# Kernel tuning notes

Measured on AMD Instinct MI355X. Metric: run time of the kernel, lower is better.

## Reference

```python
import jax, jax.numpy as jnp
import numpy as np

B, S, H = 4, 512, 1024
E, K, I = 8, 2, 2048

def setup_inputs() -> dict:
    key = jax.random.key(0)
    k1, k2, k3, k4, k5 = jax.random.split(key, 5)
    scale_h = 1.0 / np.sqrt(H)
    scale_i = 1.0 / np.sqrt(I)
    return {
        "hidden_states": jax.random.normal(k1, (B, S, H), dtype=jnp.float32),
        "router_w": jax.random.normal(k2, (E, H), dtype=jnp.float32) * scale_h,
        "w_gate": jax.random.normal(k3, (E, H, I), dtype=jnp.float32) * scale_h,
        "w_up": jax.random.normal(k4, (E, H, I), dtype=jnp.float32) * scale_h,
        "w_down": jax.random.normal(k5, (E, I, H), dtype=jnp.float32) * scale_i,
    }

def reference(hidden_states, router_w, w_gate, w_up, w_down):
    b, s, h = hidden_states.shape
    x = hidden_states.reshape(-1, h)              # [T, H] tokens
    T = x.shape[0]

    # ---- RouterTopK: fp32 linear -> softmax over all experts -> top-k ----
    router_logits = x.astype(jnp.float32) @ router_w.T          # [T, E]
    probs = jax.nn.softmax(router_logits, axis=-1)               # [T, E]
    top_vals, top_idx = jax.lax.top_k(probs, K)                  # [T, K]

    # normalize_top_k_affinities (norm_topk_prob=True)
    top_vals = top_vals / jnp.sum(top_vals, axis=-1, keepdims=True)

    # scatter normalized affinities into a dense [T, E] combine matrix
    aff = jnp.zeros((T, E), dtype=x.dtype).at[jnp.arange(T)[:, None], top_idx].set(top_vals.astype(x.dtype))

    # ---- ExpertMLPs: GLU (swiglu) per expert, combine weighted by affinity ----
    # Dense-per-expert computation; non-selected experts contribute 0 via aff.
    gate = jnp.einsum('th,ehi->eti', x, w_gate)                  # [E, T, I]
    up = jnp.einsum('th,ehi->eti', x, w_up)                      # [E, T, I]
    act = jax.nn.silu(gate) * up                                 # [E, T, I]
    expert_out = jnp.einsum('eti,eih->eth', act, w_down)         # [E, T, H]
    out = jnp.einsum('eth,te->th', expert_out, aff)              # [T, H]

    # _reduce_output: all-reduce over TP/world group -> identity single-device
    return out.reshape(b, s, h)
```

## Files before the change

### kernel.cpp

```cpp
#include <hip/hip_runtime.h>
#include <hip/hip_bf16.h>

#define T_TOK 2048
#define H_DIM 1024
#define E_N   8
#define I_DIM 2048

#define NT_MAX 40
#define MAX_SLOTS 5120

typedef unsigned short u16;
typedef unsigned int   u32;
typedef __bf16 bf16_t;
typedef bf16_t bf16x8 __attribute__((ext_vector_type(8)));
typedef u16    u16x8  __attribute__((ext_vector_type(8)));
typedef float  f32x4  __attribute__((ext_vector_type(4)));

#define MFMA __builtin_amdgcn_mfma_f32_16x16x32_bf16

__device__ __forceinline__ u16 bfbits(float f) {
    bf16_t b = (bf16_t)f;
    return __builtin_bit_cast(u16, b);
}

__device__ __forceinline__ int bt_off(int n, int kb) {
    return n * 72 + ((kb ^ ((n >> 2) & 7)) << 3);
}

__global__ __launch_bounds__(64) void router_k(
    const float* __restrict__ x, const float* __restrict__ rw,
    int* __restrict__ cnt, int* __restrict__ tok, float* __restrict__ wts,
    u16* __restrict__ xbf)
{
    int t = blockIdx.x;
    int lane = threadIdx.x;
    const float* xr = x + (size_t)t * H_DIM;
    u16* xbr = xbf + (size_t)t * H_DIM;

    float acc[E_N];
#pragma unroll
    for (int e = 0; e < E_N; e++) acc[e] = 0.f;
    for (int j = 0; j < H_DIM / 64; j++) {
        float xv = xr[lane + 64 * j];
        xbr[lane + 64 * j] = bfbits(xv);
#pragma unroll
        for (int e = 0; e < E_N; e++)
            acc[e] += xv * rw[e * H_DIM + lane + 64 * j];
    }
#pragma unroll
    for (int e = 0; e < E_N; e++) {
        float v = acc[e];
        for (int off = 32; off; off >>= 1) v += __shfl_xor(v, off);
        acc[e] = v;
    }
    if (lane == 0) {
        int i0 = 0; float m0 = acc[0];
#pragma unroll
        for (int e = 1; e < E_N; e++) if (acc[e] > m0) { m0 = acc[e]; i0 = e; }
        int i1 = -1; float m1 = -INFINITY;
#pragma unroll
        for (int e = 0; e < E_N; e++) if (e != i0 && acc[e] > m1) { m1 = acc[e]; i1 = e; }
        float w0 = 1.f / (1.f + expf(m1 - m0));
        float w1 = 1.f - w0;
        int p0 = atomicAdd(&cnt[i0], 1);
        tok[i0 * T_TOK + p0] = t; wts[i0 * T_TOK + p0] = w0;
        int p1 = atomicAdd(&cnt[i1], 1);
        tok[i1 * T_TOK + p1] = t; wts[i1 * T_TOK + p1] = w1;
    }
}

__global__ void prefix_k(const int* __restrict__ cnt, int* __restrict__ offs_pad,
                         int* __restrict__ tile_e, int* __restrict__ tile_row0,
                         int* __restrict__ ntiles)
{
    if (threadIdx.x == 0) {
        int s = 0, nt = 0;
        for (int e = 0; e < E_N; e++) {
            offs_pad[e] = s;
            int c = cnt[e];
            int t = (c + 127) >> 7;
            for (int i = 0; i < t; i++) { tile_e[nt] = e; tile_row0[nt] = i * 128; nt++; }
            s += t * 128;
        }
        offs_pad[E_N] = s;
        *ntiles = nt;
    }
}

__global__ __launch_bounds__(256, 2) void gateup_k(
    const u16* __restrict__ xbf, const float* __restrict__ wg, const float* __restrict__ wu,
    const int* __restrict__ cnt, const int* __restrict__ offs_pad,
    const int* __restrict__ tile_e, const int* __restrict__ tile_row0,
    const int* __restrict__ ntiles, const int* __restrict__ tok,
    u16* __restrict__ act)
{
    int q = gridDim.x >> 3;
    int phys = blockIdx.x;
    int logical = (phys & 7) * q + (phys >> 3);
    int tb = logical % NT_MAX;
    int n0 = (logical / NT_MAX) * 128;
    if (tb >= *ntiles) return;
    int e = tile_e[tb], row0 = tile_row0[tb];
    int cntE = cnt[e];
    int slot0 = offs_pad[e] + row0;

    __shared__ u16 BT[2][2][128 * 72];

    int tid = threadIdx.x;
    int lane = tid & 63, wid = tid >> 6;
    int wm = wid >> 1, wn = wid & 1;
    int l15 = lane & 15, lg = lane >> 4;

    const u16* arow[4];
#pragma unroll
    for (int mf = 0; mf < 4; mf++) {
        int rr = row0 + wm * 64 + mf * 16 + l15;
        int rc = rr < cntE ? rr : cntE - 1;
        arow[mf] = xbf + (size_t)tok[e * T_TOK + rc] * H_DIM;
    }

    int nq = tid & 31;
    int kb = tid >> 5;
    int sn = nq * 4;

    const float* gptr = wg + ((size_t)e * H_DIM + kb * 8) * I_DIM + n0 + sn;
    const float* uptr = wu + ((size_t)e * H_DIM + kb * 8) * I_DIM + n0 + sn;

    float4 vg[8], vu[8];
#pragma unroll
    for (int i = 0; i < 8; i++) {
        vg[i] = *reinterpret_cast<const float4*>(gptr + (size_t)i * I_DIM);
        vu[i] = *reinterpret_cast<const float4*>(uptr + (size_t)i * I_DIM);
    }

    f32x4 accg[4][4], accu[4][4];
#pragma unroll
    for (int a = 0; a < 4; a++)
#pragma unroll
        for (int b = 0; b < 4; b++) { accg[a][b] = (f32x4)0.f; accu[a][b] = (f32x4)0.f; }

    for (int k0 = 0; k0 < H_DIM; k0 += 64) {
        int buf = (k0 >> 6) & 1;
#pragma unroll
        for (int c = 0; c < 4; c++) {
            u16x8 p;
#pragma unroll
            for (int i = 0; i < 8; i++) {
                float f = (c == 0) ? vg[i].x : (c == 1) ? vg[i].y : (c == 2) ? vg[i].z : vg[i].w;
                p[i] = bfbits(f);
            }
            *reinterpret_cast<u16x8*>(&BT[buf][0][bt_off(sn + c, kb)]) = p;
        }
#pragma unroll
        for (int c = 0; c < 4; c++) {
            u16x8 p;
#pragma unroll
            for (int i = 0; i < 8; i++) {
                float f = (c == 0) ? vu[i].x : (c == 1) ? vu[i].y : (c == 2) ? vu[i].z : vu[i].w;
                p[i] = bfbits(f);
            }
            *reinterpret_cast<u16x8*>(&BT[buf][1][bt_off(sn + c, kb)]) = p;
        }
        if (k0 + 64 < H_DIM) {
#pragma unroll
            for (int i = 0; i < 8; i++) {
                vg[i] = *reinterpret_cast<const float4*>(gptr + (size_t)(k0 + 64 + i) * I_DIM);
                vu[i] = *reinterpret_cast<const float4*>(uptr + (size_t)(k0 + 64 + i) * I_DIM);
            }
        }
        __syncthreads();

#pragma unroll
        for (int ks = 0; ks < 2; ks++) {
            bf16x8 af[4];
#pragma unroll
            for (int mf = 0; mf < 4; mf++)
                af[mf] = *reinterpret_cast<const bf16x8*>(arow[mf] + k0 + ks * 32 + lg * 8);
            int kbr = ks * 4 + lg;
#pragma unroll
            for (int nf = 0; nf < 4; nf++) {
                int c = wn * 64 + nf * 16 + l15;
                bf16x8 bg = *reinterpret_cast<const bf16x8*>(&BT[buf][0][bt_off(c, kbr)]);
                bf16x8 bu = *reinterpret_cast<const bf16x8*>(&BT[buf][1][bt_off(c, kbr)]);
#pragma unroll
                for (int mf = 0; mf < 4; mf++) {
                    accg[mf][nf] = MFMA(af[mf], bg, accg[mf][nf], 0, 0, 0);
                    accu[mf][nf] = MFMA(af[mf], bu, accu[mf][nf], 0, 0, 0);
                }
            }
        }
    }

#pragma unroll
    for (int mf = 0; mf < 4; mf++)
#pragma unroll
        for (int j = 0; j < 4; j++) {
            int rl = wm * 64 + mf * 16 + lg * 4 + j;
            bool valid = (row0 + rl) < cntE;
            size_t base = (size_t)(slot0 + rl) * I_DIM + n0;
#pragma unroll
            for (int nf = 0; nf < 4; nf++) {
                float g = accg[mf][nf][j];
                float u = accu[mf][nf][j];
                float a = valid ? (g / (1.f + expf(-g))) * u : 0.f;
                act[base + wn * 64 + nf * 16 + l15] = bfbits(a);
            }
        }
}

__global__ __launch_bounds__(256, 2) void down_k(
    const u16* __restrict__ act, const float* __restrict__ wd,
    const int* __restrict__ cnt, const int* __restrict__ offs_pad,
    const int* __restrict__ tile_e, const int* __restrict__ tile_row0,
    const int* __restrict__ ntiles, const int* __restrict__ tok,
    const float* __restrict__ wts, float* __restrict__ out)
{
    int q = gridDim.x >> 3;
    int phys = blockIdx.x;
    int logical = (phys & 7) * q + (phys >> 3);
    int tb = logical % NT_MAX;
    int h0 = (logical / NT_MAX) * 128;
    if (tb >= *ntiles) return;
    int e = tile_e[tb], row0 = tile_row0[tb];
    int cntE = cnt[e];
    int slot0 = offs_pad[e] + row0;

    __shared__ u16 BT[2][128 * 72];

    int tid = threadIdx.x;
    int lane = tid & 63, wid = tid >> 6;
    int wm = wid >> 1, wn = wid & 1;
    int l15 = lane & 15, lg = lane >> 4;

    const u16* arow[4];
#pragma unroll
    for (int mf = 0; mf < 4; mf++)
        arow[mf] = act + (size_t)(slot0 + wm * 64 + mf * 16 + l15) * I_DIM;

    int nq = tid & 31;
    int kb = tid >> 5;
    int sn = nq * 4;

    const float* dptr = wd + ((size_t)e * I_DIM + kb * 8) * H_DIM + h0 + sn;

    float4 vd[8];
#pragma unroll
    for (int i = 0; i < 8; i++)
        vd[i] = *reinterpret_cast<const float4*>(dptr + (size_t)i * H_DIM);

    f32x4 acc[4][4];
#pragma unroll
    for (int a = 0; a < 4; a++)
#pragma unroll
        for (int b = 0; b < 4; b++) acc[a][b] = (f32x4)0.f;

    for (int k0 = 0; k0 < I_DIM; k0 += 64) {
        int buf = (k0 >> 6) & 1;
#pragma unroll
        for (int c = 0; c < 4; c++) {
            u16x8 p;
#pragma unroll
            for (int i = 0; i < 8; i++) {
                float f = (c == 0) ? vd[i].x : (c == 1) ? vd[i].y : (c == 2) ? vd[i].z : vd[i].w;
                p[i] = bfbits(f);
            }
            *reinterpret_cast<u16x8*>(&BT[buf][bt_off(sn + c, kb)]) = p;
        }
        if (k0 + 64 < I_DIM) {
#pragma unroll
            for (int i = 0; i < 8; i++)
                vd[i] = *reinterpret_cast<const float4*>(dptr + (size_t)(k0 + 64 + i) * H_DIM);
        }
        __syncthreads();

#pragma unroll
        for (int ks = 0; ks < 2; ks++) {
            bf16x8 af[4];
#pragma unroll
            for (int mf = 0; mf < 4; mf++)
                af[mf] = *reinterpret_cast<const bf16x8*>(arow[mf] + k0 + ks * 32 + lg * 8);
            int kbr = ks * 4 + lg;
#pragma unroll
            for (int nf = 0; nf < 4; nf++) {
                int c = wn * 64 + nf * 16 + l15;
                bf16x8 bfr = *reinterpret_cast<const bf16x8*>(&BT[buf][bt_off(c, kbr)]);
#pragma unroll
                for (int mf = 0; mf < 4; mf++)
                    acc[mf][nf] = MFMA(af[mf], bfr, acc[mf][nf], 0, 0, 0);
            }
        }
    }

#pragma unroll
    for (int mf = 0; mf < 4; mf++)
#pragma unroll
        for (int j = 0; j < 4; j++) {
            int rl = wm * 64 + mf * 16 + lg * 4 + j;
            int gr = row0 + rl;
            if (gr < cntE) {
                float w = wts[e * T_TOK + gr];
                int t   = tok[e * T_TOK + gr];
                size_t base = (size_t)t * H_DIM + h0;
#pragma unroll
                for (int nf = 0; nf < 4; nf++)
                    atomicAdd(&out[base + wn * 64 + nf * 16 + l15], acc[mf][nf][j] * w);
            }
        }
}

extern "C" void kernel_launch(void* const* d_in, const int* in_sizes, int n_in,
                              void* d_out, int out_size, void* d_ws, size_t ws_size,
                              hipStream_t stream)
{
    const float* x  = (const float*)d_in[0];
    const float* rw = (const float*)d_in[1];
    const float* wg = (const float*)d_in[2];
    const float* wu = (const float*)d_in[3];
    const float* wd = (const float*)d_in[4];
    float* out = (float*)d_out;

    char* ws = (char*)d_ws;
    int*   cnt       = (int*)(ws);
    int*   ntiles    = (int*)(ws + 32);
    int*   offs_pad  = (int*)(ws + 64);
    int*   tile_e    = (int*)(ws + 256);
    int*   tile_row0 = (int*)(ws + 512);
    int*   tok       = (int*)(ws + 64 * 1024);
    float* wts       = (float*)(ws + 128 * 1024);
    u16*   xbf       = (u16*)(ws + 256 * 1024);
    u16*   act       = (u16*)(ws + 4608 * 1024);

    size_t need = 4608ull * 1024 + (size_t)MAX_SLOTS * I_DIM * 2;
    if (ws_size < need) return;

    hipMemsetAsync(cnt, 0, 32, stream);
    hipMemsetAsync(out, 0, (size_t)T_TOK * H_DIM * sizeof(float), stream);

    router_k<<<T_TOK, 64, 0, stream>>>(x, rw, cnt, tok, wts, xbf);
    prefix_k<<<1, 64, 0, stream>>>(cnt, offs_pad, tile_e, tile_row0, ntiles);
    gateup_k<<<NT_MAX * (I_DIM / 128), 256, 0, stream>>>(
        xbf, wg, wu, cnt, offs_pad, tile_e, tile_row0, ntiles, tok, act);
    down_k<<<NT_MAX * (H_DIM / 128), 256, 0, stream>>>(
        act, wd, cnt, offs_pad, tile_e, tile_row0, ntiles, tok, wts, out);
}
```

Measured before the change: 245.7 us.

## Pre-convert weights to swizzled bf16 tiles and stream via global_load_lds

A new prep kernel converts all fp32 expert weights into pre-swizzled bf16 tiles in workspace each call, alongside the router work. The GEMM kernels then stage both A rows and weight tiles directly into LDS with global_load_lds double buffering and explicit waitcnt/barriers. They also move to 512-thread blocks with smaller per-wave M tiles, and the down projection is split along K into two halves. This removes the in-loop fp32 load and convert from the GEMMs, at the cost of an extra full pass over the weights (read fp32, write bf16) and twice as many atomic adds into the output.

```diff
diff --git a/kernel.cpp b/kernel.cpp
--- a/kernel.cpp
+++ b/kernel.cpp
@@ -23,49 +23,101 @@
     return __builtin_bit_cast(u16, b);
 }
 
-__device__ __forceinline__ int bt_off(int n, int kb) {
-    return n * 72 + ((kb ^ ((n >> 2) & 7)) << 3);
-}
-
-__global__ __launch_bounds__(64) void router_k(
+__device__ __forceinline__ void gload_lds16(const void* g, void* l) {
+    __builtin_amdgcn_global_load_lds(
+        (const __attribute__((address_space(1))) void*)g,
+        (__attribute__((address_space(3))) void*)l, 16, 0, 0);
+}
+
+__device__ __forceinline__ int tile_off(int n, int kb) {
+    return n * 64 + ((kb ^ ((n >> 1) & 7)) << 3);
+}
+__device__ __forceinline__ int a_off(int row, int kslot) {
+    return row * 64 + ((kslot ^ (row & 7)) << 3);
+}
+
+__global__ __launch_bounds__(256) void prep_k(
     const float* __restrict__ x, const float* __restrict__ rw,
+    const float* __restrict__ wg, const float* __restrict__ wu, const float* __restrict__ wd,
+    u16* __restrict__ tg, u16* __restrict__ tu, u16* __restrict__ td,
     int* __restrict__ cnt, int* __restrict__ tok, float* __restrict__ wts,
     u16* __restrict__ xbf)
 {
-    int t = blockIdx.x;
-    int lane = threadIdx.x;
-    const float* xr = x + (size_t)t * H_DIM;
-    u16* xbr = xbf + (size_t)t * H_DIM;
-
-    float acc[E_N];
-#pragma unroll
-    for (int e = 0; e < E_N; e++) acc[e] = 0.f;
-    for (int j = 0; j < H_DIM / 64; j++) {
-        float xv = xr[lane + 64 * j];
-        xbr[lane + 64 * j] = bfbits(xv);
-#pragma unroll
-        for (int e = 0; e < E_N; e++)
-            acc[e] += xv * rw[e * H_DIM + lane + 64 * j];
-    }
-#pragma unroll
-    for (int e = 0; e < E_N; e++) {
-        float v = acc[e];
-        for (int off = 32; off; off >>= 1) v += __shfl_xor(v, off);
-        acc[e] = v;
-    }
-    if (lane == 0) {
-        int i0 = 0; float m0 = acc[0];
-#pragma unroll
-        for (int e = 1; e < E_N; e++) if (acc[e] > m0) { m0 = acc[e]; i0 = e; }
-        int i1 = -1; float m1 = -INFINITY;
-#pragma unroll
-        for (int e = 0; e < E_N; e++) if (e != i0 && acc[e] > m1) { m1 = acc[e]; i1 = e; }
-        float w0 = 1.f / (1.f + expf(m1 - m0));
-        float w1 = 1.f - w0;
-        int p0 = atomicAdd(&cnt[i0], 1);
-        tok[i0 * T_TOK + p0] = t; wts[i0 * T_TOK + p0] = w0;
-        int p1 = atomicAdd(&cnt[i1], 1);
-        tok[i1 * T_TOK + p1] = t; wts[i1 * T_TOK + p1] = w1;
+    __shared__ float S[64][132];
+    int bid = blockIdx.x;
+
+    if (bid >= 6144) {
+        int wid = threadIdx.x >> 6, lane = threadIdx.x & 63;
+        int t = (bid - 6144) * 4 + wid;
+        const float* xr = x + (size_t)t * H_DIM;
+        u16* xbr = xbf + (size_t)t * H_DIM;
+        float acc[E_N];
+#pragma unroll
+        for (int e = 0; e < E_N; e++) acc[e] = 0.f;
+        for (int j = 0; j < H_DIM / 64; j++) {
+            float xv = xr[lane + 64 * j];
+            xbr[lane + 64 * j] = bfbits(xv);
+#pragma unroll
+            for (int e = 0; e < E_N; e++)
+                acc[e] += xv * rw[e * H_DIM + lane + 64 * j];
+        }
+#pragma unroll
+        for (int e = 0; e < E_N; e++) {
+            float v = acc[e];
+            for (int off = 32; off; off >>= 1) v += __shfl_xor(v, off);
+            acc[e] = v;
+        }
+        if (lane == 0) {
+            int i0 = 0; float m0 = acc[0];
+#pragma unroll
+            for (int e = 1; e < E_N; e++) if (acc[e] > m0) { m0 = acc[e]; i0 = e; }
+            int i1 = -1; float m1 = -INFINITY;
+#pragma unroll
+            for (int e = 0; e < E_N; e++) if (e != i0 && acc[e] > m1) { m1 = acc[e]; i1 = e; }
+            float w0 = 1.f / (1.f + expf(m1 - m0));
+            float w1 = 1.f - w0;
+            int p0 = atomicAdd(&cnt[i0], 1);
+            tok[i0 * T_TOK + p0] = t; wts[i0 * T_TOK + p0] = w0;
+            int p1 = atomicAdd(&cnt[i1], 1);
+            tok[i1 * T_TOK + p1] = t; wts[i1 * T_TOK + p1] = w1;
+        }
+        return;
+    }
+
+    int kind = bid >> 11;
+    int ti = bid & 2047;
+    const float* src; u16* dst; int nstr;
+    if (kind < 2) {
+        const float* w = kind ? wu : wg;
+        int e = ti >> 8, b = ti & 15;
+        int p = (ti >> 4) & 15;
+        src = w + ((size_t)e * H_DIM + b * 64) * I_DIM + p * 128;
+        nstr = I_DIM;
+        dst = (kind ? tu : tg) + (size_t)ti * 8192;
+    } else {
+        int e = ti >> 8, r = ti & 255;
+        int p = r >> 5, b = r & 31;
+        src = wd + ((size_t)e * I_DIM + b * 64) * H_DIM + p * 128;
+        nstr = H_DIM;
+        dst = td + (size_t)ti * 8192;
+    }
+    int tid = threadIdx.x;
+#pragma unroll
+    for (int i = 0; i < 8; i++) {
+        int idx = tid + i * 256;
+        int k = idx >> 5, c4 = idx & 31;
+        float4 v = *reinterpret_cast<const float4*>(src + (size_t)k * nstr + c4 * 4);
+        *reinterpret_cast<float4*>(&S[k][c4 * 4]) = v;
+    }
+    __syncthreads();
+#pragma unroll
+    for (int i = 0; i < 4; i++) {
+        int oidx = tid + i * 256;
+        int n = oidx & 127, kb = oidx >> 7;
+        u16x8 pk;
+#pragma unroll
+        for (int j = 0; j < 8; j++) pk[j] = bfbits(S[kb * 8 + j][n]);
+        *reinterpret_cast<u16x8*>(dst + tile_off(n, kb)) = pk;
     }
 }
 
@@ -87,8 +139,8 @@
     }
 }
 
-__global__ __launch_bounds__(256, 2) void gateup_k(
-    const u16* __restrict__ xbf, const float* __restrict__ wg, const float* __restrict__ wu,
+__global__ __launch_bounds__(512, 2) void gateup_k(
+    const u16* __restrict__ xbf, const u16* __restrict__ tg, const u16* __restrict__ tu,
     const int* __restrict__ cnt, const int* __restrict__ offs_pad,
     const int* __restrict__ tile_e, const int* __restrict__ tile_row0,
     const int* __restrict__ ntiles, const int* __restrict__ tok,
@@ -98,104 +150,90 @@
     int phys = blockIdx.x;
     int logical = (phys & 7) * q + (phys >> 3);
     int tb = logical % NT_MAX;
-    int n0 = (logical / NT_MAX) * 128;
+    int p  = logical / NT_MAX;
     if (tb >= *ntiles) return;
     int e = tile_e[tb], row0 = tile_row0[tb];
     int cntE = cnt[e];
     int slot0 = offs_pad[e] + row0;
-
-    __shared__ u16 BT[2][2][128 * 72];
+    int n0 = p * 128;
+
+    __shared__ u16 AS[2][8192], GS[2][8192], US[2][8192];
 
     int tid = threadIdx.x;
     int lane = tid & 63, wid = tid >> 6;
-    int wm = wid >> 1, wn = wid & 1;
+    int wm = wid & 3, wn = wid >> 2;
     int l15 = lane & 15, lg = lane >> 4;
 
-    const u16* arow[4];
-#pragma unroll
-    for (int mf = 0; mf < 4; mf++) {
-        int rr = row0 + wm * 64 + mf * 16 + l15;
-        int rc = rr < cntE ? rr : cntE - 1;
-        arow[mf] = xbf + (size_t)tok[e * T_TOK + rc] * H_DIM;
-    }
-
-    int nq = tid & 31;
-    int kb = tid >> 5;
-    int sn = nq * 4;
-
-    const float* gptr = wg + ((size_t)e * H_DIM + kb * 8) * I_DIM + n0 + sn;
-    const float* uptr = wu + ((size_t)e * H_DIM + kb * 8) * I_DIM + n0 + sn;
-
-    float4 vg[8], vu[8];
-#pragma unroll
-    for (int i = 0; i < 8; i++) {
-        vg[i] = *reinterpret_cast<const float4*>(gptr + (size_t)i * I_DIM);
-        vu[i] = *reinterpret_cast<const float4*>(uptr + (size_t)i * I_DIM);
-    }
-
-    f32x4 accg[4][4], accu[4][4];
-#pragma unroll
-    for (int a = 0; a < 4; a++)
+    const u16* asrc[2];
+#pragma unroll
+    for (int i = 0; i < 2; i++) {
+        int row = (wid * 2 + i) * 8 + (lane >> 3);
+        int rc = (row0 + row < cntE) ? (row0 + row) : (cntE - 1);
+        asrc[i] = xbf + (size_t)tok[e * T_TOK + rc] * H_DIM + (((lane & 7) ^ (lane >> 3)) << 3);
+    }
+    const u16* tgB = tg + ((size_t)(e * 16 + p) * 16) * 8192;
+    const u16* tuB = tu + ((size_t)(e * 16 + p) * 16) * 8192;
+    int s0 = (wid * 2) * 512;
+
+#define STAGE_GU(bufi, t) { \
+    gload_lds16(asrc[0] + (size_t)(t) * 64, &AS[bufi][s0]); \
+    gload_lds16(asrc[1] + (size_t)(t) * 64, &AS[bufi][s0 + 512]); \
+    gload_lds16(tgB + (size_t)(t) * 8192 + s0 + lane * 8,       &GS[bufi][s0]); \
+    gload_lds16(tgB + (size_t)(t) * 8192 + s0 + 512 + lane * 8, &GS[bufi][s0 + 512]); \
+    gload_lds16(tuB + (size_t)(t) * 8192 + s0 + lane * 8,       &US[bufi][s0]); \
+    gload_lds16(tuB + (size_t)(t) * 8192 + s0 + 512 + lane * 8, &US[bufi][s0 + 512]); }
+
+    f32x4 accg[2][4], accu[2][4];
+#pragma unroll
+    for (int a = 0; a < 2; a++)
 #pragma unroll
         for (int b = 0; b < 4; b++) { accg[a][b] = (f32x4)0.f; accu[a][b] = (f32x4)0.f; }
 
-    for (int k0 = 0; k0 < H_DIM; k0 += 64) {
-        int buf = (k0 >> 6) & 1;
-#pragma unroll
-        for (int c = 0; c < 4; c++) {
-            u16x8 p;
-#pragma unroll
-            for (int i = 0; i < 8; i++) {
-                float f = (c == 0) ? vg[i].x : (c == 1) ? vg[i].y : (c == 2) ? vg[i].z : vg[i].w;
-                p[i] = bfbits(f);
-            }
-            *reinterpret_cast<u16x8*>(&BT[buf][0][bt_off(sn + c, kb)]) = p;
-        }
-#pragma unroll
-        for (int c = 0; c < 4; c++) {
-            u16x8 p;
-#pragma unroll
-            for (int i = 0; i < 8; i++) {
-                float f = (c == 0) ? vu[i].x : (c == 1) ? vu[i].y : (c == 2) ? vu[i].z : vu[i].w;
-                p[i] = bfbits(f);
-            }
-            *reinterpret_cast<u16x8*>(&BT[buf][1][bt_off(sn + c, kb)]) = p;
-        }
-        if (k0 + 64 < H_DIM) {
-#pragma unroll
-            for (int i = 0; i < 8; i++) {
-                vg[i] = *reinterpret_cast<const float4*>(gptr + (size_t)(k0 + 64 + i) * I_DIM);
-                vu[i] = *reinterpret_cast<const float4*>(uptr + (size_t)(k0 + 64 + i) * I_DIM);
-            }
-        }
-        __syncthreads();
+    STAGE_GU(0, 0);
+
+    for (int t = 0; t < 16; t++) {
+        int buf = t & 1;
+        if (t + 1 < 16) {
+            STAGE_GU(buf ^ 1, t + 1);
+            asm volatile("s_waitcnt vmcnt(6)" ::: "memory");
+        } else {
+            asm volatile("s_waitcnt vmcnt(0)" ::: "memory");
+        }
+        __builtin_amdgcn_s_barrier();
+        __builtin_amdgcn_sched_barrier(0);
 
 #pragma unroll
         for (int ks = 0; ks < 2; ks++) {
-            bf16x8 af[4];
-#pragma unroll
-            for (int mf = 0; mf < 4; mf++)
-                af[mf] = *reinterpret_cast<const bf16x8*>(arow[mf] + k0 + ks * 32 + lg * 8);
+            bf16x8 af[2];
+#pragma unroll
+            for (int mf = 0; mf < 2; mf++) {
+                int row = wm * 32 + mf * 16 + l15;
+                af[mf] = *reinterpret_cast<const bf16x8*>(&AS[buf][a_off(row, ks * 4 + lg)]);
+            }
             int kbr = ks * 4 + lg;
 #pragma unroll
             for (int nf = 0; nf < 4; nf++) {
                 int c = wn * 64 + nf * 16 + l15;
-                bf16x8 bg = *reinterpret_cast<const bf16x8*>(&BT[buf][0][bt_off(c, kbr)]);
-                bf16x8 bu = *reinterpret_cast<const bf16x8*>(&BT[buf][1][bt_off(c, kbr)]);
-#pragma unroll
-                for (int mf = 0; mf < 4; mf++) {
+                int o = tile_off(c, kbr);
+                bf16x8 bg = *reinterpret_cast<const bf16x8*>(&GS[buf][o]);
+                bf16x8 bu = *reinterpret_cast<const bf16x8*>(&US[buf][o]);
+#pragma unroll
+                for (int mf = 0; mf < 2; mf++) {
                     accg[mf][nf] = MFMA(af[mf], bg, accg[mf][nf], 0, 0, 0);
                     accu[mf][nf] = MFMA(af[mf], bu, accu[mf][nf], 0, 0, 0);
                 }
             }
         }
-    }
-
-#pragma unroll
-    for (int mf = 0; mf < 4; mf++)
+        __builtin_amdgcn_s_barrier();
+        __builtin_amdgcn_sched_barrier(0);
+    }
+#undef STAGE_GU
+
+#pragma unroll
+    for (int mf = 0; mf < 2; mf++)
 #pragma unroll
         for (int j = 0; j < 4; j++) {
-            int rl = wm * 64 + mf * 16 + lg * 4 + j;
+            int rl = wm * 32 + mf * 16 + lg * 4 + j;
             bool valid = (row0 + rl) < cntE;
             size_t base = (size_t)(slot0 + rl) * I_DIM + n0;
 #pragma unroll
@@ -208,8 +246,8 @@
         }
 }
 
-__global__ __launch_bounds__(256, 2) void down_k(
-    const u16* __restrict__ act, const float* __restrict__ wd,
+__global__ __launch_bounds__(512, 4) void down_k(
+    const u16* __restrict__ act, const u16* __restrict__ td,
     const int* __restrict__ cnt, const int* __restrict__ offs_pad,
     const int* __restrict__ tile_e, const int* __restrict__ tile_row0,
     const int* __restrict__ ntiles, const int* __restrict__ tok,
@@ -219,83 +257,85 @@
     int phys = blockIdx.x;
     int logical = (phys & 7) * q + (phys >> 3);
     int tb = logical % NT_MAX;
-    int h0 = (logical / NT_MAX) * 128;
+    int rest = logical / NT_MAX;
+    int p  = rest & 7;
+    int kh = rest >> 3;
     if (tb >= *ntiles) return;
     int e = tile_e[tb], row0 = tile_row0[tb];
     int cntE = cnt[e];
     int slot0 = offs_pad[e] + row0;
-
-    __shared__ u16 BT[2][128 * 72];
+    int h0 = p * 128;
+
+    __shared__ u16 AS[2][8192], DS[2][8192];
 
     int tid = threadIdx.x;
     int lane = tid & 63, wid = tid >> 6;
-    int wm = wid >> 1, wn = wid & 1;
+    int wm = wid & 3, wn = wid >> 2;
     int l15 = lane & 15, lg = lane >> 4;
 
-    const u16* arow[4];
-#pragma unroll
-    for (int mf = 0; mf < 4; mf++)
-        arow[mf] = act + (size_t)(slot0 + wm * 64 + mf * 16 + l15) * I_DIM;
-
-    int nq = tid & 31;
-    int kb = tid >> 5;
-    int sn = nq * 4;
-
-    const float* dptr = wd + ((size_t)e * I_DIM + kb * 8) * H_DIM + h0 + sn;
-
-    float4 vd[8];
-#pragma unroll
-    for (int i = 0; i < 8; i++)
-        vd[i] = *reinterpret_cast<const float4*>(dptr + (size_t)i * H_DIM);
-
-    f32x4 acc[4][4];
-#pragma unroll
-    for (int a = 0; a < 4; a++)
+    const u16* asrc[2];
+#pragma unroll
+    for (int i = 0; i < 2; i++) {
+        int row = (wid * 2 + i) * 8 + (lane >> 3);
+        asrc[i] = act + (size_t)(slot0 + row) * I_DIM + kh * 1024
+                  + (((lane & 7) ^ (lane >> 3)) << 3);
+    }
+    const u16* tdB = td + ((size_t)(e * 8 + p) * 32 + kh * 16) * 8192;
+    int s0 = (wid * 2) * 512;
+
+#define STAGE_D(bufi, t) { \
+    gload_lds16(asrc[0] + (size_t)(t) * 64, &AS[bufi][s0]); \
+    gload_lds16(asrc[1] + (size_t)(t) * 64, &AS[bufi][s0 + 512]); \
+    gload_lds16(tdB + (size_t)(t) * 8192 + s0 + lane * 8,       &DS[bufi][s0]); \
+    gload_lds16(tdB + (size_t)(t) * 8192 + s0 + 512 + lane * 8, &DS[bufi][s0 + 512]); }
+
+    f32x4 acc[2][4];
+#pragma unroll
+    for (int a = 0; a < 2; a++)
 #pragma unroll
         for (int b = 0; b < 4; b++) acc[a][b] = (f32x4)0.f;
 
-    for (int k0 = 0; k0 < I_DIM; k0 += 64) {
-        int buf = (k0 >> 6) & 1;
-#pragma unroll
-        for (int c = 0; c < 4; c++) {
-            u16x8 p;
-#pragma unroll
-            for (int i = 0; i < 8; i++) {
-                float f = (c == 0) ? vd[i].x : (c == 1) ? vd[i].y : (c == 2) ? vd[i].z : vd[i].w;
-                p[i] = bfbits(f);
-            }
-            *reinterpret_cast<u16x8*>(&BT[buf][bt_off(sn + c, kb)]) = p;
-        }
-        if (k0 + 64 < I_DIM) {
-#pragma unroll
-            for (int i = 0; i < 8; i++)
-                vd[i] = *reinterpret_cast<const float4*>(dptr + (size_t)(k0 + 64 + i) * H_DIM);
-        }
-        __syncthreads();
+    STAGE_D(0, 0);
+
+    for (int t = 0; t < 16; t++) {
+        int buf = t & 1;
+        if (t + 1 < 16) {
+            STAGE_D(buf ^ 1, t + 1);
+            asm volatile("s_waitcnt vmcnt(4)" ::: "memory");
+        } else {
+            asm volatile("s_waitcnt vmcnt(0)" ::: "memory");
+        }
+        __builtin_amdgcn_s_barrier();
+        __builtin_amdgcn_sched_barrier(0);
 
 #pragma unroll
         for (int ks = 0; ks < 2; ks++) {
-            bf16x8 af[4];
-#pragma unroll
-            for (int mf = 0; mf < 4; mf++)
-                af[mf] = *reinterpret_cast<const bf16x8*>(arow[mf] + k0 + ks * 32 + lg * 8);
+            bf16x8 af[2];
+#pragma unroll
+            for (int mf = 0; mf < 2; mf++) {
+                int row = wm * 32 + mf * 16 + l15;
+                af[mf] = *reinterpret_cast<const bf16x8*>(&AS[buf][a_off(row, ks * 4 + lg)]);
+            }
             int kbr = ks * 4 + lg;
 #pragma unroll
             for (int nf = 0; nf < 4; nf++) {
                 int c = wn * 64 + nf * 16 + l15;
-                bf16x8 bfr = *reinterpret_cast<const bf16x8*>(&BT[buf][bt_off(c, kbr)]);
-#pragma unroll
-                for (int mf = 0; mf < 4; mf++)
-                    acc[mf][nf] = MFMA(af[mf], bfr, acc[mf][nf], 0, 0, 0);
-            }
-        }
-    }
-
-#pragma unroll
-    for (int mf = 0; mf < 4; mf++)
+                bf16x8 bd = *reinterpret_cast<const bf16x8*>(&DS[buf][tile_off(c, kbr)]);
+#pragma unroll
+                for (int mf = 0; mf < 2; mf++)
+                    acc[mf][nf] = MFMA(af[mf], bd, acc[mf][nf], 0, 0, 0);
+            }
+        }
+        __builtin_amdgcn_s_barrier();
+        __builtin_amdgcn_sched_barrier(0);
+    }
+#undef STAGE_D
+
+#pragma unroll
+    for (int mf = 0; mf < 2; mf++)
 #pragma unroll
         for (int j = 0; j < 4; j++) {
-            int rl = wm * 64 + mf * 16 + lg * 4 + j;
+            int rl = wm * 32 + mf * 16 + lg * 4 + j;
             int gr = row0 + rl;
             if (gr < cntE) {
                 float w = wts[e * T_TOK + gr];
@@ -330,16 +370,23 @@
     u16*   xbf       = (u16*)(ws + 256 * 1024);
     u16*   act       = (u16*)(ws + 4608 * 1024);
 
-    size_t need = 4608ull * 1024 + (size_t)MAX_SLOTS * I_DIM * 2;
+    const size_t OFF_TG = 28ull << 20;
+    const size_t TSZ    = 2048ull * 16384;
+    u16* tg = (u16*)(ws + OFF_TG);
+    u16* tu = (u16*)(ws + OFF_TG + TSZ);
+    u16* td = (u16*)(ws + OFF_TG + 2 * TSZ);
+
+    size_t need = OFF_TG + 3 * TSZ;
     if (ws_size < need) return;
 
     hipMemsetAsync(cnt, 0, 32, stream);
     hipMemsetAsync(out, 0, (size_t)T_TOK * H_DIM * sizeof(float), stream);
 
-    router_k<<<T_TOK, 64, 0, stream>>>(x, rw, cnt, tok, wts, xbf);
+    prep_k<<<6144 + T_TOK / 4, 256, 0, stream>>>(x, rw, wg, wu, wd, tg, tu, td,
+                                                 cnt, tok, wts, xbf);
     prefix_k<<<1, 64, 0, stream>>>(cnt, offs_pad, tile_e, tile_row0, ntiles);
-    gateup_k<<<NT_MAX * (I_DIM / 128), 256, 0, stream>>>(
-        xbf, wg, wu, cnt, offs_pad, tile_e, tile_row0, ntiles, tok, act);
-    down_k<<<NT_MAX * (H_DIM / 128), 256, 0, stream>>>(
-        act, wd, cnt, offs_pad, tile_e, tile_row0, ntiles, tok, wts, out);
-}
+    gateup_k<<<NT_MAX * (I_DIM / 128), 512, 0, stream>>>(
+        xbf, tg, tu, cnt, offs_pad, tile_e, tile_row0, ntiles, tok, act);
+    down_k<<<NT_MAX * (H_DIM / 128) * 2, 512, 0, stream>>>(
+        act, td, cnt, offs_pad, tile_e, tile_row0, ntiles, tok, wts, out);
+}
```

New measurement: 238.7 us. 2.8% less time.
